# Optimization experiments

Measured on AMD Instinct MI355X. Metric: run time of the kernel, lower is better.

## Reference

```python
import jax, jax.numpy as jnp
import numpy as np

EPS = 1e-5
LEAK = 0.1

def conv2d(x, w, b, stride, pad):
    y = jax.lax.conv_general_dilated(
        x, w, (stride, stride), ((pad, pad), (pad, pad)),
        dimension_numbers=('NCHW', 'OIHW', 'NCHW'))
    return y + b[None, :, None, None]

def batchnorm_train(x, gamma, beta):
    # torch BatchNorm2d in training mode: biased batch stats over (N,H,W)
    mean = x.mean(axis=(0, 2, 3), keepdims=True)
    var = x.var(axis=(0, 2, 3), keepdims=True)
    xn = (x - mean) * jax.lax.rsqrt(var + EPS)
    return xn * gamma[None, :, None, None] + beta[None, :, None, None]

def se_block(x, w1, w2):
    y = x.mean(axis=(2, 3))              # (B,C)
    y = jax.nn.relu(y @ w1.T)            # (B,C//r)
    y = jax.nn.sigmoid(y @ w2.T)         # (B,C)
    return x * y[:, :, None, None]

def haar_dwt2(x):
    # level-1 2D Haar DWT on last two (even) axes; matches pywt 'haar' for even sizes
    a = x[..., ::2, ::2]; b = x[..., ::2, 1::2]
    c = x[..., 1::2, ::2]; d = x[..., 1::2, 1::2]
    cA = (a + b + c + d) * 0.5
    cH = (a + b - c - d) * 0.5
    cV = (a - b + c - d) * 0.5
    cD = (a - b - c + d) * 0.5
    return cA, cH, cV, cD

def haar_idwt2(cA, cH, cV, cD):
    a = (cA + cH + cV + cD) * 0.5
    b = (cA + cH - cV - cD) * 0.5
    c = (cA - cH + cV - cD) * 0.5
    d = (cA - cH - cV + cD) * 0.5
    B, C, h, w = cA.shape
    out = jnp.zeros((B, C, 2 * h, 2 * w), cA.dtype)
    out = out.at[..., ::2, ::2].set(a)
    out = out.at[..., ::2, 1::2].set(b)
    out = out.at[..., 1::2, ::2].set(c)
    out = out.at[..., 1::2, 1::2].set(d)
    return out


def setup_inputs() -> dict:
    key = jax.random.key(0)
    ks = jax.random.split(key, 16)
    ndf = 18
    inp = {}
    inp['x'] = jax.random.normal(ks[0], (16, 3, 510, 510), jnp.float32)
    inp['conv1_w'] = jax.random.normal(ks[1], (ndf, 3, 4, 4), jnp.float32) * 0.05
    inp['conv1_b'] = jnp.zeros((ndf,), jnp.float32)
    inp['bn1_g'] = jnp.ones((ndf,), jnp.float32)
    inp['bn1_b'] = jnp.zeros((ndf,), jnp.float32)
    inp['se1_w1'] = jax.random.normal(ks[2], (ndf // 16, ndf), jnp.float32) * 0.1
    inp['se1_w2'] = jax.random.normal(ks[3], (ndf, ndf // 16), jnp.float32) * 0.1
    inp['conv2_w'] = jax.random.normal(ks[4], (2 * ndf, ndf, 3, 3), jnp.float32) * 0.05
    inp['conv2_b'] = jnp.zeros((2 * ndf,), jnp.float32)
    inp['bn2_g'] = jnp.ones((2 * ndf,), jnp.float32)
    inp['bn2_b'] = jnp.zeros((2 * ndf,), jnp.float32)
    inp['se2_w1'] = jax.random.normal(ks[5], (2 * ndf // 16, 2 * ndf), jnp.float32) * 0.1
    inp['se2_w2'] = jax.random.normal(ks[6], (2 * ndf, 2 * ndf // 16), jnp.float32) * 0.1
    # review_module's per-forward Conv2d(ndf -> 2*ndf, k=1), frozen as fixed random params
    inp['review_w'] = jax.random.normal(ks[7], (2 * ndf, ndf), jnp.float32) * 0.1
    inp['review_b'] = jnp.zeros((2 * ndf,), jnp.float32)
    inp['final_w'] = jax.random.normal(ks[8], (2, 2 * ndf), jnp.float32) * 0.1
    inp['final_b'] = jnp.zeros((2,), jnp.float32)
    return inp


def reference(x, conv1_w, conv1_b, bn1_g, bn1_b, se1_w1, se1_w2,
              conv2_w, conv2_b, bn2_g, bn2_b, se2_w1, se2_w2,
              review_w, review_b, final_w, final_b):
    # enc1: conv4 s2 p2 + BN + LeakyReLU(0.1)
    x1 = jax.nn.leaky_relu(batchnorm_train(conv2d(x, conv1_w, conv1_b, 2, 2), bn1_g, bn1_b), LEAK)
    x1_se = se_block(x1, se1_w1, se1_w2)
    # enc2: conv3 s1 p1 + BN + LeakyReLU(0.1)
    x2 = jax.nn.leaky_relu(batchnorm_train(conv2d(x1_se, conv2_w, conv2_b, 1, 1), bn2_g, bn2_b), LEAK)
    x2 = se_block(x2, se2_w1, se2_w2)

    # dwt_transform detaches -> stop_gradient to mirror torch .detach()
    x2_c = haar_dwt2(jax.lax.stop_gradient(x2))

    # review_module: 1x1 conv + relu on stage 'enc1' output (pre-SE x1)
    reviewed = jax.nn.relu(jnp.einsum('bchw,oc->bohw', x1, review_w) + review_b[None, :, None, None])
    # F.interpolate(nearest) to x2 spatial size: identity here (enc2 is stride-1)
    r_c = haar_dwt2(jax.lax.stop_gradient(reviewed))

    # add in frequency domain, then inverse transform
    summed = tuple(a + b for a, b in zip(x2_c, r_c))
    x2_recon = haar_idwt2(*summed)

    pooled = x2_recon.mean(axis=(2, 3))           # (B, 2*ndf)
    out = pooled @ final_w.T + final_b            # (B, 2)
    return (x2, out)
```

## Files before the change

### kernel.cpp

```cpp
#include <hip/hip_runtime.h>
#include <math.h>

#define B     16
#define C0    3
#define H0    510
#define W0    510
#define C1    18
#define C2    36
#define H     256
#define W     256
#define HW    65536
#define NSTAT 1048576
#define EPS   1e-5f
#define LEAK  0.1f

#define X1_FLOATS   18874368
#define OFF_BN1_SUM   0
#define OFF_BN1_SQ    18
#define OFF_POOL1     72
#define OFF_S1        360
#define OFF_BN2_SUM   648
#define OFF_BN2_SQ    684
#define OFF_POOL2     792
#define OFF_S2        1368
#define OFF_REVSUM    1944
#define STATS_TOTAL   2520

#define OUT_X2_FLOATS 37748736

__device__ inline float wave_reduce_sum(float v) {
  #pragma unroll
  for (int off = 32; off > 0; off >>= 1) v += __shfl_down(v, off, 64);
  return v;
}

template<int NCH>
__device__ inline void block_stats(const float* acc, float* gsum, float* gsq) {
  __shared__ float smem_s[4][NCH];
  __shared__ float smem_q[4][NCH];
  const int tid = threadIdx.x, wave = tid >> 6, lane = tid & 63;
  #pragma unroll
  for (int o = 0; o < NCH; ++o) {
    float s = wave_reduce_sum(acc[o]);
    float q = wave_reduce_sum(acc[o] * acc[o]);
    if (lane == 0) { smem_s[wave][o] = s; smem_q[wave][o] = q; }
  }
  __syncthreads();
  if (tid < NCH) {
    atomicAdd(&gsum[tid], smem_s[0][tid] + smem_s[1][tid] + smem_s[2][tid] + smem_s[3][tid]);
    atomicAdd(&gsq[tid],  smem_q[0][tid] + smem_q[1][tid] + smem_q[2][tid] + smem_q[3][tid]);
  }
}

__global__ __launch_bounds__(256) void conv1_kernel(
    const float* __restrict__ x, const float* __restrict__ w,
    const float* __restrict__ bias, float* __restrict__ out,
    float* __restrict__ gsum, float* __restrict__ gsq)
{
  const int b = blockIdx.z;
  const int tid = threadIdx.x;
  const int ly = tid >> 4, lx = tid & 15;
  const int oy = blockIdx.y * 16 + ly;
  const int ox = blockIdx.x * 16 + lx;

  float acc[C1];
  #pragma unroll
  for (int o = 0; o < C1; ++o) acc[o] = bias[o];

  const float* xb = x + (size_t)b * C0 * H0 * W0;
  const bool interior = (blockIdx.x >= 1) && (blockIdx.x <= 14) &&
                        (blockIdx.y >= 1) && (blockIdx.y <= 14);

  if (interior) {
    const float* xp = xb + (oy * 2 - 2) * W0 + (ox * 2 - 2);
    #pragma unroll
    for (int c = 0; c < C0; ++c) {
      float iv[16];
      #pragma unroll
      for (int ky = 0; ky < 4; ++ky)
        #pragma unroll
        for (int kx = 0; kx < 4; ++kx)
          iv[ky * 4 + kx] = xp[c * (H0 * W0) + ky * W0 + kx];
      #pragma unroll
      for (int o = 0; o < C1; ++o) {
        float a = acc[o];
        #pragma unroll
        for (int t = 0; t < 16; ++t) a = fmaf(iv[t], w[o * 48 + c * 16 + t], a);
        acc[o] = a;
      }
    }
  } else {
    #pragma unroll
    for (int c = 0; c < C0; ++c) {
      float iv[16];
      #pragma unroll
      for (int ky = 0; ky < 4; ++ky) {
        const int iy = oy * 2 - 2 + ky;
        #pragma unroll
        for (int kx = 0; kx < 4; ++kx) {
          const int ix = ox * 2 - 2 + kx;
          const bool ok = (iy >= 0) && (iy < H0) && (ix >= 0) && (ix < W0);
          iv[ky * 4 + kx] = ok ? xb[c * (H0 * W0) + iy * W0 + ix] : 0.0f;
        }
      }
      #pragma unroll
      for (int o = 0; o < C1; ++o) {
        float a = acc[o];
        #pragma unroll
        for (int t = 0; t < 16; ++t) a = fmaf(iv[t], w[o * 48 + c * 16 + t], a);
        acc[o] = a;
      }
    }
  }

  float* ob = out + ((size_t)b * C1) * HW + oy * W + ox;
  #pragma unroll
  for (int o = 0; o < C1; ++o) ob[(size_t)o * HW] = acc[o];

  block_stats<C1>(acc, gsum, gsq);
}

__global__ __launch_bounds__(256) void bnpool_kernel(
    const float* __restrict__ buf, const float* __restrict__ stats,
    int sum_off, int sq_off,
    const float* __restrict__ g, const float* __restrict__ be,
    float* __restrict__ pool, int nch)
{
  const int c = blockIdx.y, b = blockIdx.z;
  const int tid = threadIdx.x;
  const float inv_n = 1.0f / (float)NSTAT;
  const float mean = stats[sum_off + c] * inv_n;
  const float var  = stats[sq_off + c] * inv_n - mean * mean;
  const float sc   = g[c] * rsqrtf(var + EPS);
  const float sh   = be[c] - mean * sc;

  const float* p = buf + ((size_t)(b * nch + c)) * HW + blockIdx.x * 8192 + tid * 4;
  float acc = 0.0f;
  #pragma unroll
  for (int k = 0; k < 8; ++k) {
    float4 v = *(const float4*)(p + k * 1024);
    float r0 = fmaf(v.x, sc, sh); r0 = r0 > 0.0f ? r0 : LEAK * r0;
    float r1 = fmaf(v.y, sc, sh); r1 = r1 > 0.0f ? r1 : LEAK * r1;
    float r2 = fmaf(v.z, sc, sh); r2 = r2 > 0.0f ? r2 : LEAK * r2;
    float r3 = fmaf(v.w, sc, sh); r3 = r3 > 0.0f ? r3 : LEAK * r3;
    acc += (r0 + r1) + (r2 + r3);
  }

  float s = wave_reduce_sum(acc);
  __shared__ float smem[4];
  const int wave = tid >> 6, lane = tid & 63;
  if (lane == 0) smem[wave] = s;
  __syncthreads();
  if (tid == 0) atomicAdd(&pool[b * nch + c], smem[0] + smem[1] + smem[2] + smem[3]);
}

__global__ void se1_kernel(float* __restrict__ stats,
                           const float* __restrict__ w1, const float* __restrict__ w2)
{
  __shared__ float hid[B];
  const int t = threadIdx.x;
  if (t < B) {
    float h = 0.0f;
    for (int c = 0; c < C1; ++c)
      h += stats[OFF_POOL1 + t * C1 + c] * (1.0f / (float)HW) * w1[c];
    hid[t] = fmaxf(h, 0.0f);
  }
  __syncthreads();
  for (int i = t; i < B * C1; i += 64) {
    const int b = i / C1, c = i % C1;
    const float v = hid[b] * w2[c];
    stats[OFF_S1 + i] = 1.0f / (1.0f + expf(-v));
  }
}

__global__ __launch_bounds__(256, 6) void conv2_kernel(
    const float* __restrict__ x1raw, const float* __restrict__ w,
    const float* __restrict__ bias, const float* __restrict__ stats,
    const float* __restrict__ bn1_g, const float* __restrict__ bn1_b,
    const float* __restrict__ s1,
    const float* __restrict__ rw, const float* __restrict__ rb,
    float* __restrict__ out, float* __restrict__ gsum, float* __restrict__ gsq,
    float* __restrict__ revsum)
{
  __shared__ float in_lds[C1 * 18 * 18];
  __shared__ float bn1sc[C1], bn1sh[C1];
  __shared__ float red_s[4][18];
  __shared__ float red_q[4][18];
  __shared__ float red_r[4][18];

  const int b = blockIdx.z;
  const int ty0 = blockIdx.y * 16, tx0 = blockIdx.x * 16;
  const int tid = threadIdx.x;

  if (tid < C1) {
    const float inv_n = 1.0f / (float)NSTAT;
    const float mean = stats[OFF_BN1_SUM + tid] * inv_n;
    const float var  = stats[OFF_BN1_SQ + tid] * inv_n - mean * mean;
    const float sc   = bn1_g[tid] * rsqrtf(var + EPS);
    bn1sc[tid] = sc;
    bn1sh[tid] = bn1_b[tid] - mean * sc;
  }
  __syncthreads();

  const float* xb = x1raw + (size_t)b * C1 * HW;
  for (int i = tid; i < C1 * 324; i += 256) {
    const int c = i / 324;
    const int rem = i - c * 324;
    const int r = rem / 18;
    const int col = rem - r * 18;
    const int gy = ty0 - 1 + r;
    const int gx = tx0 - 1 + col;
    float v = 0.0f;
    if (gy >= 0 && gy < H && gx >= 0 && gx < W) {
      v = fmaf(xb[c * HW + gy * W + gx], bn1sc[c], bn1sh[c]);
      v = v > 0.0f ? v : LEAK * v;
    }
    in_lds[i] = v;
  }
  __syncthreads();

  const int ly = tid >> 4, lx = tid & 15;
  const int wave = tid >> 6, lane = tid & 63;
  const float* s1b = s1 + b * C1;

  #pragma unroll 1
  for (int p = 0; p < 2; ++p) {
    const int ob18 = p * 18;
    float acc[18], racc[18], cent[C1];
    #pragma unroll
    for (int j = 0; j < 18; ++j) { acc[j] = bias[ob18 + j]; racc[j] = rb[ob18 + j]; }

    for (int c = 0; c < C1; ++c) {
      float iv[9];
      #pragma unroll
      for (int ky = 0; ky < 3; ++ky)
        #pragma unroll
        for (int kx = 0; kx < 3; ++kx)
          iv[ky * 3 + kx] = in_lds[c * 324 + (ly + ky) * 18 + (lx + kx)];

      cent[c] = iv[4];
      const float s1c = s1b[c];
      #pragma unroll
      for (int t = 0; t < 9; ++t) iv[t] *= s1c;

      const float* wc = w + (size_t)ob18 * 162 + c * 9;
      #pragma unroll
      for (int j = 0; j < 18; ++j) {
        #pragma unroll
        for (int t = 0; t < 9; ++t)
          acc[j] = fmaf(iv[t], wc[j * 162 + t], acc[j]);
      }
    }

    #pragma unroll
    for (int j = 0; j < 18; ++j) {
      const float* rr = rw + (size_t)(ob18 + j) * C1;
      float r = racc[j];
      #pragma unroll
      for (int c = 0; c < C1; ++c) r = fmaf(cent[c], rr[c], r);
      racc[j] = r;
    }

    float* ob = out + ((size_t)(b * C2 + ob18)) * HW + (ty0 + ly) * W + tx0 + lx;
    #pragma unroll
    for (int j = 0; j < 18; ++j) ob[(size_t)j * HW] = acc[j];

    __syncthreads();
    #pragma unroll
    for (int j = 0; j < 18; ++j) {
      float s  = wave_reduce_sum(acc[j]);
      float qq = wave_reduce_sum(acc[j] * acc[j]);
      float rs = wave_reduce_sum(fmaxf(racc[j], 0.0f));
      if (lane == 0) { red_s[wave][j] = s; red_q[wave][j] = qq; red_r[wave][j] = rs; }
    }
    __syncthreads();
    if (tid < 18) {
      atomicAdd(&gsum[ob18 + tid], red_s[0][tid] + red_s[1][tid] + red_s[2][tid] + red_s[3][tid]);
      atomicAdd(&gsq[ob18 + tid],  red_q[0][tid] + red_q[1][tid] + red_q[2][tid] + red_q[3][tid]);
      atomicAdd(&revsum[b * C2 + ob18 + tid],
                red_r[0][tid] + red_r[1][tid] + red_r[2][tid] + red_r[3][tid]);
    }
  }
}

__global__ void se2_kernel(float* __restrict__ stats,
                           const float* __restrict__ w1, const float* __restrict__ w2)
{
  __shared__ float hid[B][2];
  const int t = threadIdx.x;
  if (t < B * 2) {
    const int b = t >> 1, j = t & 1;
    float h = 0.0f;
    for (int c = 0; c < C2; ++c)
      h += stats[OFF_POOL2 + b * C2 + c] * (1.0f / (float)HW) * w1[j * C2 + c];
    hid[b][j] = fmaxf(h, 0.0f);
  }
  __syncthreads();
  for (int i = t; i < B * C2; i += 64) {
    const int b = i / C2, c = i % C2;
    const float v = hid[b][0] * w2[c * 2 + 0] + hid[b][1] * w2[c * 2 + 1];
    stats[OFF_S2 + i] = 1.0f / (1.0f + expf(-v));
  }
}

__global__ __launch_bounds__(256) void apply2_kernel(
    float* __restrict__ buf, const float* __restrict__ stats,
    const float* __restrict__ g, const float* __restrict__ be,
    const float* __restrict__ s2)
{
  const int c = blockIdx.y, b = blockIdx.z;
  const int tid = threadIdx.x;
  const float inv_n = 1.0f / (float)NSTAT;
  const float mean = stats[OFF_BN2_SUM + c] * inv_n;
  const float var  = stats[OFF_BN2_SQ + c] * inv_n - mean * mean;
  const float sc   = g[c] * rsqrtf(var + EPS);
  const float sh   = be[c] - mean * sc;
  const float s    = s2[b * C2 + c];

  float* p = buf + ((size_t)(b * C2 + c)) * HW + blockIdx.x * 4096 + tid * 4;
  #pragma unroll
  for (int k = 0; k < 4; ++k) {
    float4 v = *(const float4*)(p + k * 1024);
    float r0 = fmaf(v.x, sc, sh); r0 = (r0 > 0.0f ? r0 : LEAK * r0) * s;
    float r1 = fmaf(v.y, sc, sh); r1 = (r1 > 0.0f ? r1 : LEAK * r1) * s;
    float r2 = fmaf(v.z, sc, sh); r2 = (r2 > 0.0f ? r2 : LEAK * r2) * s;
    float r3 = fmaf(v.w, sc, sh); r3 = (r3 > 0.0f ? r3 : LEAK * r3) * s;
    *(float4*)(p + k * 1024) = make_float4(r0, r1, r2, r3);
  }
}

__global__ void final_kernel(const float* __restrict__ stats,
                             const float* __restrict__ fw, const float* __restrict__ fb,
                             float* __restrict__ out)
{
  const int t = threadIdx.x;
  if (t < B * 2) {
    const int b = t >> 1, j = t & 1;
    float acc = fb[j];
    for (int o = 0; o < C2; ++o) {
      const float m = (stats[OFF_POOL2 + b * C2 + o] * stats[OFF_S2 + b * C2 + o]
                       + stats[OFF_REVSUM + b * C2 + o]) * (1.0f / (float)HW);
      acc = fmaf(m, fw[j * C2 + o], acc);
    }
    out[b * 2 + j] = acc;
  }
}

extern "C" void kernel_launch(void* const* d_in, const int* in_sizes, int n_in,
                              void* d_out, int out_size, void* d_ws, size_t ws_size,
                              hipStream_t stream) {
  const float* x        = (const float*)d_in[0];
  const float* conv1_w  = (const float*)d_in[1];
  const float* conv1_b  = (const float*)d_in[2];
  const float* bn1_g    = (const float*)d_in[3];
  const float* bn1_b    = (const float*)d_in[4];
  const float* se1_w1   = (const float*)d_in[5];
  const float* se1_w2   = (const float*)d_in[6];
  const float* conv2_w  = (const float*)d_in[7];
  const float* conv2_b  = (const float*)d_in[8];
  const float* bn2_g    = (const float*)d_in[9];
  const float* bn2_b    = (const float*)d_in[10];
  const float* se2_w1   = (const float*)d_in[11];
  const float* se2_w2   = (const float*)d_in[12];
  const float* review_w = (const float*)d_in[13];
  const float* review_b = (const float*)d_in[14];
  const float* final_w  = (const float*)d_in[15];
  const float* final_b  = (const float*)d_in[16];

  float* ws    = (float*)d_ws;
  float* x1buf = ws;
  float* stats = ws + X1_FLOATS;
  float* out   = (float*)d_out;

  hipMemsetAsync(stats, 0, STATS_TOTAL * sizeof(float), stream);

  conv1_kernel<<<dim3(16, 16, B), 256, 0, stream>>>(
      x, conv1_w, conv1_b, x1buf, stats + OFF_BN1_SUM, stats + OFF_BN1_SQ);

  bnpool_kernel<<<dim3(8, C1, B), 256, 0, stream>>>(
      x1buf, stats, OFF_BN1_SUM, OFF_BN1_SQ, bn1_g, bn1_b, stats + OFF_POOL1, C1);

  se1_kernel<<<1, 64, 0, stream>>>(stats, se1_w1, se1_w2);

  conv2_kernel<<<dim3(16, 16, B), 256, 0, stream>>>(
      x1buf, conv2_w, conv2_b, stats, bn1_g, bn1_b, stats + OFF_S1,
      review_w, review_b,
      out, stats + OFF_BN2_SUM, stats + OFF_BN2_SQ, stats + OFF_REVSUM);

  bnpool_kernel<<<dim3(8, C2, B), 256, 0, stream>>>(
      out, stats, OFF_BN2_SUM, OFF_BN2_SQ, bn2_g, bn2_b, stats + OFF_POOL2, C2);

  se2_kernel<<<1, 64, 0, stream>>>(stats, se2_w1, se2_w2);

  apply2_kernel<<<dim3(16, C2, B), 256, 0, stream>>>(
      out, stats, bn2_g, bn2_b, stats + OFF_S2);

  final_kernel<<<1, 64, 0, stream>>>(stats, final_w, final_b, out + OUT_X2_FLOATS);
}
```

Baseline: 806.8 us.

## Compute all conv2 output channels in one pass and split review into own kernel

The conv2 kernel now accumulates all 36 output channels in registers in a single pass over the LDS tile. Previously it made two passes of 18 channels each, recomputing the input window loads and scaling per pass. The review 1x1 conv and its pooled sums move to a separate kernel that rereads x1 from global memory. The shared reduction buffers reuse the input LDS tile. This cuts redundant LDS reads and per-pass sync and reduction overhead, and lowers register pressure from the fused review path. The cost is higher accumulator register use (36 live values) and an extra pass over x1 memory.

```diff
diff --git a/kernel.cpp b/kernel.cpp
--- a/kernel.cpp
+++ b/kernel.cpp
@@ -52,6 +52,21 @@
   }
 }
 
+template<int NCH>
+__device__ inline void block_reduce_sums(const float* acc, float* gout) {
+  __shared__ float smem[4][NCH];
+  const int tid = threadIdx.x, wave = tid >> 6, lane = tid & 63;
+  #pragma unroll
+  for (int o = 0; o < NCH; ++o) {
+    float s = wave_reduce_sum(acc[o]);
+    if (lane == 0) smem[wave][o] = s;
+  }
+  __syncthreads();
+  if (tid < NCH) {
+    atomicAdd(&gout[tid], smem[0][tid] + smem[1][tid] + smem[2][tid] + smem[3][tid]);
+  }
+}
+
 __global__ __launch_bounds__(256) void conv1_kernel(
     const float* __restrict__ x, const float* __restrict__ w,
     const float* __restrict__ bias, float* __restrict__ out,
@@ -178,15 +193,12 @@
     const float* __restrict__ bias, const float* __restrict__ stats,
     const float* __restrict__ bn1_g, const float* __restrict__ bn1_b,
     const float* __restrict__ s1,
-    const float* __restrict__ rw, const float* __restrict__ rb,
-    float* __restrict__ out, float* __restrict__ gsum, float* __restrict__ gsq,
-    float* __restrict__ revsum)
+    float* __restrict__ out, float* __restrict__ gsum, float* __restrict__ gsq)
 {
   __shared__ float in_lds[C1 * 18 * 18];
   __shared__ float bn1sc[C1], bn1sh[C1];
-  __shared__ float red_s[4][18];
-  __shared__ float red_q[4][18];
-  __shared__ float red_r[4][18];
+  float* red_s = in_lds;
+  float* red_q = in_lds + 144;
 
   const int b = blockIdx.z;
   const int ty0 = blockIdx.y * 16, tx0 = blockIdx.x * 16;
@@ -223,64 +235,91 @@
   const int wave = tid >> 6, lane = tid & 63;
   const float* s1b = s1 + b * C1;
 
-  #pragma unroll 1
-  for (int p = 0; p < 2; ++p) {
-    const int ob18 = p * 18;
-    float acc[18], racc[18], cent[C1];
-    #pragma unroll
-    for (int j = 0; j < 18; ++j) { acc[j] = bias[ob18 + j]; racc[j] = rb[ob18 + j]; }
-
-    for (int c = 0; c < C1; ++c) {
-      float iv[9];
-      #pragma unroll
-      for (int ky = 0; ky < 3; ++ky)
-        #pragma unroll
-        for (int kx = 0; kx < 3; ++kx)
-          iv[ky * 3 + kx] = in_lds[c * 324 + (ly + ky) * 18 + (lx + kx)];
-
-      cent[c] = iv[4];
-      const float s1c = s1b[c];
-      #pragma unroll
-      for (int t = 0; t < 9; ++t) iv[t] *= s1c;
-
-      const float* wc = w + (size_t)ob18 * 162 + c * 9;
-      #pragma unroll
-      for (int j = 0; j < 18; ++j) {
-        #pragma unroll
-        for (int t = 0; t < 9; ++t)
-          acc[j] = fmaf(iv[t], wc[j * 162 + t], acc[j]);
-      }
+  float acc[C2];
+  #pragma unroll
+  for (int j = 0; j < C2; ++j) acc[j] = bias[j];
+
+  for (int c = 0; c < C1; ++c) {
+    float iv[9];
+    #pragma unroll
+    for (int ky = 0; ky < 3; ++ky)
+      #pragma unroll
+      for (int kx = 0; kx < 3; ++kx)
+        iv[ky * 3 + kx] = in_lds[c * 324 + (ly + ky) * 18 + (lx + kx)];
+
+    const float s1c = s1b[c];
+    #pragma unroll
+    for (int t = 0; t < 9; ++t) iv[t] *= s1c;
+
+    const float* wc = w + c * 9;
+    #pragma unroll
+    for (int j = 0; j < C2; ++j) {
+      float a = acc[j];
+      #pragma unroll
+      for (int t = 0; t < 9; ++t)
+        a = fmaf(iv[t], wc[j * 162 + t], a);
+      acc[j] = a;
     }
-
-    #pragma unroll
-    for (int j = 0; j < 18; ++j) {
-      const float* rr = rw + (size_t)(ob18 + j) * C1;
-      float r = racc[j];
-      #pragma unroll
-      for (int c = 0; c < C1; ++c) r = fmaf(cent[c], rr[c], r);
-      racc[j] = r;
-    }
-
-    float* ob = out + ((size_t)(b * C2 + ob18)) * HW + (ty0 + ly) * W + tx0 + lx;
-    #pragma unroll
-    for (int j = 0; j < 18; ++j) ob[(size_t)j * HW] = acc[j];
-
-    __syncthreads();
-    #pragma unroll
-    for (int j = 0; j < 18; ++j) {
-      float s  = wave_reduce_sum(acc[j]);
-      float qq = wave_reduce_sum(acc[j] * acc[j]);
-      float rs = wave_reduce_sum(fmaxf(racc[j], 0.0f));
-      if (lane == 0) { red_s[wave][j] = s; red_q[wave][j] = qq; red_r[wave][j] = rs; }
-    }
-    __syncthreads();
-    if (tid < 18) {
-      atomicAdd(&gsum[ob18 + tid], red_s[0][tid] + red_s[1][tid] + red_s[2][tid] + red_s[3][tid]);
-      atomicAdd(&gsq[ob18 + tid],  red_q[0][tid] + red_q[1][tid] + red_q[2][tid] + red_q[3][tid]);
-      atomicAdd(&revsum[b * C2 + ob18 + tid],
-                red_r[0][tid] + red_r[1][tid] + red_r[2][tid] + red_r[3][tid]);
-    }
-  }
+  }
+
+  float* ob = out + ((size_t)b * C2) * HW + (ty0 + ly) * W + tx0 + lx;
+  #pragma unroll
+  for (int j = 0; j < C2; ++j) ob[(size_t)j * HW] = acc[j];
+
+  __syncthreads();
+  #pragma unroll
+  for (int j = 0; j < C2; ++j) {
+    float s  = wave_reduce_sum(acc[j]);
+    float qq = wave_reduce_sum(acc[j] * acc[j]);
+    if (lane == 0) { red_s[wave * 36 + j] = s; red_q[wave * 36 + j] = qq; }
+  }
+  __syncthreads();
+  if (tid < C2) {
+    atomicAdd(&gsum[tid], red_s[tid] + red_s[36 + tid] + red_s[72 + tid] + red_s[108 + tid]);
+    atomicAdd(&gsq[tid],  red_q[tid] + red_q[36 + tid] + red_q[72 + tid] + red_q[108 + tid]);
+  }
+}
+
+__global__ __launch_bounds__(256) void review_kernel(
+    const float* __restrict__ x1raw, const float* __restrict__ stats,
+    const float* __restrict__ bn1_g, const float* __restrict__ bn1_b,
+    const float* __restrict__ rw, const float* __restrict__ rb,
+    float* __restrict__ revsum)
+{
+  __shared__ float bn1sc[C1], bn1sh[C1];
+  const int b = blockIdx.y;
+  const int tid = threadIdx.x;
+  const int p = blockIdx.x * 256 + tid;
+
+  if (tid < C1) {
+    const float inv_n = 1.0f / (float)NSTAT;
+    const float mean = stats[OFF_BN1_SUM + tid] * inv_n;
+    const float var  = stats[OFF_BN1_SQ + tid] * inv_n - mean * mean;
+    const float sc   = bn1_g[tid] * rsqrtf(var + EPS);
+    bn1sc[tid] = sc;
+    bn1sh[tid] = bn1_b[tid] - mean * sc;
+  }
+  __syncthreads();
+
+  const float* xb = x1raw + (size_t)b * C1 * HW + p;
+  float xv[C1];
+  #pragma unroll
+  for (int c = 0; c < C1; ++c) {
+    float v = fmaf(xb[(size_t)c * HW], bn1sc[c], bn1sh[c]);
+    xv[c] = v > 0.0f ? v : LEAK * v;
+  }
+
+  float acc[C2];
+  #pragma unroll
+  for (int o = 0; o < C2; ++o) {
+    const float* rr = rw + o * C1;
+    float a = rb[o];
+    #pragma unroll
+    for (int c = 0; c < C1; ++c) a = fmaf(xv[c], rr[c], a);
+    acc[o] = fmaxf(a, 0.0f);
+  }
+
+  block_reduce_sums<C2>(acc, revsum + b * C2);
 }
 
 __global__ void se2_kernel(float* __restrict__ stats,
@@ -384,8 +423,10 @@
 
   conv2_kernel<<<dim3(16, 16, B), 256, 0, stream>>>(
       x1buf, conv2_w, conv2_b, stats, bn1_g, bn1_b, stats + OFF_S1,
-      review_w, review_b,
-      out, stats + OFF_BN2_SUM, stats + OFF_BN2_SQ, stats + OFF_REVSUM);
+      out, stats + OFF_BN2_SUM, stats + OFF_BN2_SQ);
+
+  review_kernel<<<dim3(256, B), 256, 0, stream>>>(
+      x1buf, stats, bn1_g, bn1_b, review_w, review_b, stats + OFF_REVSUM);
 
   bnpool_kernel<<<dim3(8, C2, B), 256, 0, stream>>>(
       out, stats, OFF_BN2_SUM, OFF_BN2_SQ, bn2_g, bn2_b, stats + OFF_POOL2, C2);
```

Result: slower. 831.1 us (+3.0%).
